# Kernel tuning notes

Measured on AMD Instinct MI355X. Metric: run time of the kernel, lower is better.

The kernel has to match this reference:

```python
import jax, jax.numpy as jnp
import numpy as np

EMBED = 2048
HEADS = 16
DFF = 4 * EMBED
EPS = 1e-5


def layernorm(x, g, b):
    mu = jnp.mean(x, axis=-1, keepdims=True)
    var = jnp.var(x, axis=-1, keepdims=True)
    return (x - mu) * jax.lax.rsqrt(var + EPS) * g + b


def setup_inputs() -> dict:
    key = jax.random.key(0)
    ks = jax.random.split(key, 16)
    s = 1.0 / np.sqrt(EMBED)
    sf = 1.0 / np.sqrt(DFF)
    return {
        "x": jax.random.normal(ks[0], (2, 2048, EMBED), jnp.float32),
        "Wq": jax.random.normal(ks[1], (EMBED, EMBED), jnp.float32) * s,
        "bq": jnp.zeros((EMBED,), jnp.float32),
        "Wk": jax.random.normal(ks[2], (EMBED, EMBED), jnp.float32) * s,
        "bk": jnp.zeros((EMBED,), jnp.float32),
        "Wv": jax.random.normal(ks[3], (EMBED, EMBED), jnp.float32) * s,
        "bv": jnp.zeros((EMBED,), jnp.float32),
        "Wo": jax.random.normal(ks[4], (EMBED, EMBED), jnp.float32) * s,
        "bo": jnp.zeros((EMBED,), jnp.float32),
        "g1": jnp.ones((EMBED,), jnp.float32),
        "b1": jnp.zeros((EMBED,), jnp.float32),
        "g2": jnp.ones((EMBED,), jnp.float32),
        "b2": jnp.zeros((EMBED,), jnp.float32),
        "W1": jax.random.normal(ks[5], (EMBED, DFF), jnp.float32) * s,
        "bf1": jnp.zeros((DFF,), jnp.float32),
        "W2": jax.random.normal(ks[6], (DFF, EMBED), jnp.float32) * sf,
        "bf2": jnp.zeros((EMBED,), jnp.float32),
    }


def reference(x, Wq, bq, Wk, bk, Wv, bv, Wo, bo, g1, b1, g2, b2, W1, bf1, W2, bf2):
    B, N, C = x.shape
    H = HEADS
    hd = C // H
    # QKV projections -> [B, H, N, hd]
    def split_heads(t):
        return t.reshape(B, N, H, hd).transpose(0, 2, 1, 3)
    q = split_heads(x @ Wq + bq)
    k = split_heads(x @ Wk + bk)
    v = split_heads(x @ Wv + bv)
    # scores [B, H, N, N]
    attn = jnp.einsum('bhqd,bhkd->bhqk', q, k) / np.sqrt(hd)
    attn = jax.nn.softmax(attn, axis=-1)
    out = jnp.einsum('bhqk,bhkd->bhqd', attn, v)
    out = out.transpose(0, 2, 1, 3).reshape(B, N, C)
    out = out @ Wo + bo
    h = layernorm(x + out, g1, b1)
    ff = jax.nn.gelu(h @ W1 + bf1, approximate=False) @ W2 + bf2
    return layernorm(h + ff, g2, b2)
```

## Files before the change

kernel.cpp:

```cpp
#include <hip/hip_runtime.h>
#include <math.h>

#define EMBED 2048
#define DFF   8192
#define TOK   4096
#define SEQ   2048
#define HEADS 16
#define HD    128
#define LDQ   6144

typedef __attribute__((ext_vector_type(8))) short short8;
typedef __attribute__((ext_vector_type(4))) float f32x4;

__device__ __forceinline__ unsigned short f2bf(float f) {
    unsigned int u = __float_as_uint(f);
    return (unsigned short)((u + 0x7FFFu + ((u >> 16) & 1u)) >> 16);
}
__device__ __forceinline__ float bf2f(unsigned short s) {
    return __uint_as_float(((unsigned int)s) << 16);
}
__device__ __forceinline__ float exp2_fast(float x) {
    return __builtin_amdgcn_exp2f(x);
}

__device__ __forceinline__ void async16(const void* g, void* l) {
    __builtin_amdgcn_global_load_lds((const __attribute__((address_space(1))) void*)g,
                                     (__attribute__((address_space(3))) void*)l, 16, 0, 0);
}

__device__ __forceinline__ float gelu_fast(float v) {
    const float y = 1.5957691216057308f * (v + 0.044715f * v * v * v);
    return v / (1.0f + __expf(-y));
}

template<int MODE>
__global__ __launch_bounds__(256, 2)
void gemm_bf16(const unsigned short* __restrict__ A, const unsigned short* __restrict__ B,
               const float* __restrict__ bias, const void* __restrict__ resid,
               unsigned short* __restrict__ C, int M, int N, int K, int lda)
{
    __shared__ __align__(16) float smemf[8448];
    unsigned short* As = (unsigned short*)smemf;
    unsigned short* Bs = As + 8192;
    float* Cs = smemf;

    const int t = threadIdx.x;
    const int w = t >> 6, l = t & 63;
    const int quad = l >> 4, m16 = l & 15;
    const long bm = (long)blockIdx.y * 128, bn = (long)blockIdx.x * 128;
    const int wr = (w >> 1)*64, wc = (w & 1)*64;

    f32x4 acc[4][4] = {};

    const int srow = w*16 + (l >> 2);
    const int sslot = l & 3;
    const unsigned short* Ag = A + (size_t)bm*lda;
    const unsigned short* Bg = B + (size_t)bn*K;

#pragma unroll
    for (int u = 0; u < 2; ++u) {
        const int row = u*64 + srow;
        const int c = sslot ^ ((row >> 1) & 3);
        async16(Ag + (size_t)row*lda + c*8, &As[u*2048 + w*512]);
        async16(Bg + (size_t)row*K   + c*8, &Bs[u*2048 + w*512]);
    }

    const int iters = K >> 5;
    for (int it = 0; it < iters; ++it) {
        __syncthreads();
        if (it + 1 < iters) {
            const int k0 = (it + 1) << 5;
            const int bo = ((it + 1) & 1) * 4096;
#pragma unroll
            for (int u = 0; u < 2; ++u) {
                const int row = u*64 + srow;
                const int c = sslot ^ ((row >> 1) & 3);
                async16(Ag + (size_t)row*lda + k0 + c*8, &As[bo + u*2048 + w*512]);
                async16(Bg + (size_t)row*K   + k0 + c*8, &Bs[bo + u*2048 + w*512]);
            }
        }
        const int co = (it & 1) * 4096;
        short8 af[4], bf[4];
#pragma unroll
        for (int s = 0; s < 4; ++s) {
            const int ra = wr + s*16 + m16;
            const int sla = quad ^ ((ra >> 1) & 3);
            af[s] = *(const short8*)&As[co + ra*32 + sla*8];
            const int rb = wc + s*16 + m16;
            const int slb = quad ^ ((rb >> 1) & 3);
            bf[s] = *(const short8*)&Bs[co + rb*32 + slb*8];
        }
#pragma unroll
        for (int ms = 0; ms < 4; ++ms)
#pragma unroll
            for (int ns = 0; ns < 4; ++ns)
                acc[ms][ns] = __builtin_amdgcn_mfma_f32_16x16x32_bf16(af[ms], bf[ns], acc[ms][ns], 0, 0, 0);
    }

    const int ecol = (t & 15) * 8;
    float bias8[8];
#pragma unroll
    for (int i = 0; i < 8; ++i) bias8[i] = bias[bn + ecol + i];

#pragma unroll
    for (int pass = 0; pass < 2; ++pass) {
        __syncthreads();
        if ((w >> 1) == pass) {
#pragma unroll
            for (int ms = 0; ms < 4; ++ms)
#pragma unroll
                for (int ns = 0; ns < 4; ++ns)
#pragma unroll
                    for (int r = 0; r < 4; ++r)
                        Cs[(ms*16 + quad*4 + r)*132 + wc + ns*16 + m16] = acc[ms][ns][r];
        }
        __syncthreads();
#pragma unroll
        for (int j = 0; j < 4; ++j) {
            const int row = j*16 + (t >> 4);
            float v[8];
            *(f32x4*)&v[0] = *(const f32x4*)&Cs[row*132 + ecol];
            *(f32x4*)&v[4] = *(const f32x4*)&Cs[row*132 + ecol + 4];
            const long gr = bm + pass*64 + row;
            const long go = gr*N + bn + ecol;
            float r8[8];
            if (MODE == 1) {
                *(f32x4*)&r8[0] = *(const f32x4*)((const float*)resid + go);
                *(f32x4*)&r8[4] = *(const f32x4*)((const float*)resid + go + 4);
            }
            short8 rb16;
            if (MODE == 3) rb16 = *(const short8*)((const unsigned short*)resid + go);
            short8 o;
#pragma unroll
            for (int i = 0; i < 8; ++i) {
                float y = v[i] + bias8[i];
                if (MODE == 1) y += r8[i];
                if (MODE == 3) y += bf2f((unsigned short)rb16[i]);
                if (MODE == 2) y = gelu_fast(y);
                o[i] = (short)f2bf(y);
            }
            *(short8*)&C[go] = o;
        }
    }
}

__global__ __launch_bounds__(256, 2)
void attn_flash(unsigned short* __restrict__ qkv)
{
    __shared__ unsigned short Ks2[2][64*128];
    __shared__ unsigned short Vt2[2][128*72];
    __shared__ unsigned short Ps[4*16*72];

    const int t = threadIdx.x;
    const int w = t >> 6, l = t & 63;
    const int quad = l >> 4, m16 = l & 15;

    const int dd = blockIdx.x;
    const int bh = (dd & 7)*4 + ((dd >> 3) >> 5);
    const int qt = (dd >> 3) & 31;
    const int b = bh >> 4, h = bh & 15;

    const long rowq = (long)b*SEQ + qt*64;
    const long rowb = (long)b*SEQ;
    const int qc = h*HD;
    const int kc = EMBED + h*HD;
    const int vc = 2*EMBED + h*HD;

    const int rbase = w*4 + (l >> 4);
    const int slot  = l & 15;
    const int vslot = t & 15;
    const int vrp   = t >> 4;

    unsigned short* Qs = Ks2[1];

    short8 va[2], vb[2];
#pragma unroll
    for (int u = 0; u < 2; ++u) {
        const int rp = u*16 + vrp;
        va[u] = *(const short8*)(qkv + (rowb + 2*rp    )*LDQ + vc + vslot*8);
        vb[u] = *(const short8*)(qkv + (rowb + 2*rp + 1)*LDQ + vc + vslot*8);
    }
#pragma unroll
    for (int u = 0; u < 4; ++u) {
        const int row = u*16 + rbase;
        const int c = slot ^ ((row >> 1) & 7);
        async16(qkv + (rowq + row)*LDQ + qc + c*8, Qs + u*2048 + w*512);
        async16(qkv + (rowb + row)*LDQ + kc + c*8, &Ks2[0][u*2048 + w*512]);
    }
#pragma unroll
    for (int u = 0; u < 2; ++u) {
        const int rp = u*16 + vrp;
#pragma unroll
        for (int i = 0; i < 8; ++i) {
            const int dv = vslot*8 + i;
            const int col = (2*rp) ^ (((dv >> 5) & 3) << 3);
            unsigned int pv = (unsigned int)(unsigned short)va[u][i] |
                              ((unsigned int)(unsigned short)vb[u][i] << 16);
            *(unsigned int*)&Vt2[0][dv*72 + col] = pv;
        }
    }
    __syncthreads();

    short8 af[4];
#pragma unroll
    for (int ks = 0; ks < 4; ++ks) {
        const int row = w*16 + m16;
        const int sl = (4*ks + quad) ^ ((row >> 1) & 7);
        af[ks] = *(const short8*)&Qs[row*128 + sl*8];
    }
    __syncthreads();

    f32x4 O[8] = {};
    float mrun[4] = {-1e30f,-1e30f,-1e30f,-1e30f};
    float lrun[4] = {0.f,0.f,0.f,0.f};
    unsigned short* Pw = Ps + w*16*72;
    const float SC = 0.08838834764831845f * 1.4426950408889634f;

    for (int kt = 0; kt < SEQ/64; ++kt) {
        const int cur = kt & 1;
        const bool pre = (kt + 1 < SEQ/64);
        const long rowkv = rowb + (long)(kt + 1)*64;

        if (pre) {
#pragma unroll
            for (int u = 0; u < 2; ++u) {
                const int rp = u*16 + vrp;
                va[u] = *(const short8*)(qkv + (rowkv + 2*rp    )*LDQ + vc + vslot*8);
                vb[u] = *(const short8*)(qkv + (rowkv + 2*rp + 1)*LDQ + vc + vslot*8);
            }
#pragma unroll
            for (int u = 0; u < 4; ++u) {
                const int row = u*16 + rbase;
                const int c = slot ^ ((row >> 1) & 7);
                async16(qkv + (rowkv + row)*LDQ + kc + c*8, &Ks2[cur^1][u*2048 + w*512]);
            }
        }

        f32x4 S[4];
#pragma unroll
        for (int ns = 0; ns < 4; ++ns) {
            f32x4 a = {0.f,0.f,0.f,0.f};
            const int row = ns*16 + m16;
            const int swr = (row >> 1) & 7;
#pragma unroll
            for (int ks = 0; ks < 4; ++ks) {
                const int sl = (4*ks + quad) ^ swr;
                const short8 bfr = *(const short8*)&Ks2[cur][row*128 + sl*8];
                a = __builtin_amdgcn_mfma_f32_16x16x32_bf16(af[ks], bfr, a, 0, 0, 0);
            }
#pragma unroll
            for (int r = 0; r < 4; ++r) a[r] *= SC;
            S[ns] = a;
        }

        float al[4], rs[4];
#pragma unroll
        for (int r = 0; r < 4; ++r) {
            float tm = fmaxf(fmaxf(S[0][r], S[1][r]), fmaxf(S[2][r], S[3][r]));
            tm = fmaxf(tm, __shfl_xor(tm, 1));
            tm = fmaxf(tm, __shfl_xor(tm, 2));
            tm = fmaxf(tm, __shfl_xor(tm, 4));
            tm = fmaxf(tm, __shfl_xor(tm, 8));
            const float mn = fmaxf(mrun[r], tm);
            al[r] = exp2_fast(mrun[r] - mn);
            mrun[r] = mn;
            rs[r] = 0.f;
        }
#pragma unroll
        for (int ns = 0; ns < 4; ++ns)
#pragma unroll
            for (int r = 0; r < 4; ++r) {
                const float p = exp2_fast(S[ns][r] - mrun[r]);
                rs[r] += p;
                Pw[(quad*4 + r)*72 + ns*16 + m16] = f2bf(p);
            }
#pragma unroll
        for (int r = 0; r < 4; ++r) {
            rs[r] += __shfl_xor(rs[r], 1);
            rs[r] += __shfl_xor(rs[r], 2);
            rs[r] += __shfl_xor(rs[r], 4);
            rs[r] += __shfl_xor(rs[r], 8);
            lrun[r] = lrun[r]*al[r] + rs[r];
        }
        if (__any((al[0] != 1.f) | (al[1] != 1.f) | (al[2] != 1.f) | (al[3] != 1.f))) {
#pragma unroll
            for (int i = 0; i < 8; ++i)
#pragma unroll
                for (int r = 0; r < 4; ++r) O[i][r] *= al[r];
        }

        if (pre) {
#pragma unroll
            for (int u = 0; u < 2; ++u) {
                const int rp = u*16 + vrp;
#pragma unroll
                for (int i = 0; i < 8; ++i) {
                    const int dv = vslot*8 + i;
                    const int col = (2*rp) ^ (((dv >> 5) & 3) << 3);
                    unsigned int pv = (unsigned int)(unsigned short)va[u][i] |
                                      ((unsigned int)(unsigned short)vb[u][i] << 16);
                    *(unsigned int*)&Vt2[cur^1][dv*72 + col] = pv;
                }
            }
        }

#pragma unroll
        for (int ks2 = 0; ks2 < 2; ++ks2) {
            const short8 ap = *(const short8*)&Pw[m16*72 + ks2*32 + quad*8];
#pragma unroll
            for (int ds = 0; ds < 8; ++ds) {
                const int dv = ds*16 + m16;
                const int jcol = (ks2*32 + quad*8) ^ (((dv >> 5) & 3) << 3);
                const short8 bv = *(const short8*)&Vt2[cur][dv*72 + jcol];
                O[ds] = __builtin_amdgcn_mfma_f32_16x16x32_bf16(ap, bv, O[ds], 0, 0, 0);
            }
        }

        __syncthreads();
    }

    float inv[4];
#pragma unroll
    for (int r = 0; r < 4; ++r) inv[r] = 1.0f / lrun[r];
#pragma unroll
    for (int ds = 0; ds < 8; ++ds)
#pragma unroll
        for (int r = 0; r < 4; ++r) {
            const long row = rowq + w*16 + quad*4 + r;
            qkv[row*LDQ + qc + ds*16 + m16] = f2bf(O[ds][r] * inv[r]);
        }
}

template<int OUTF32>
__global__ __launch_bounds__(256)
void ln_bf16(const unsigned short* __restrict__ X, const float* __restrict__ g,
             const float* __restrict__ be, void* __restrict__ Y)
{
    __shared__ float r1[256], r2[256];
    const int t = threadIdx.x;
    const long row = blockIdx.x;
    const unsigned short* x = X + row*EMBED;
    float v[8];
    const short8 xv = *(const short8*)(x + t*8);
    float s = 0.f, s2 = 0.f;
#pragma unroll
    for (int i = 0; i < 8; ++i) {
        v[i] = bf2f((unsigned short)xv[i]);
        s += v[i]; s2 += v[i]*v[i];
    }
    r1[t] = s; r2[t] = s2;
    __syncthreads();
    for (int k = 128; k > 0; k >>= 1) {
        if (t < k) { r1[t] += r1[t+k]; r2[t] += r2[t+k]; }
        __syncthreads();
    }
    const float mu = r1[0] * (1.0f/EMBED);
    const float var = r2[0] * (1.0f/EMBED) - mu*mu;
    const float rstd = rsqrtf(var + 1e-5f);
    if (OUTF32) {
        float* y = (float*)Y + row*EMBED + t*8;
#pragma unroll
        for (int i = 0; i < 8; ++i) y[i] = (v[i]-mu)*rstd*g[t*8+i] + be[t*8+i];
    } else {
        unsigned short* y = (unsigned short*)Y + row*EMBED;
        short8 o;
#pragma unroll
        for (int i = 0; i < 8; ++i) o[i] = (short)f2bf((v[i]-mu)*rstd*g[t*8+i] + be[t*8+i]);
        *(short8*)(y + t*8) = o;
    }
}

__global__ __launch_bounds__(256)
void cvt_transpose(const float* __restrict__ W, unsigned short* __restrict__ Wt, int K, int N)
{
    __shared__ unsigned short T[32][33];
    const int t = threadIdx.x;
    const long n0 = (long)blockIdx.x*32, k0 = (long)blockIdx.y*32;
    {
        const int r = t >> 3, c = (t & 7)*4;
        const float4 vv = *(const float4*)&W[(k0 + r)*N + n0 + c];
        T[r][c+0] = f2bf(vv.x); T[r][c+1] = f2bf(vv.y);
        T[r][c+2] = f2bf(vv.z); T[r][c+3] = f2bf(vv.w);
    }
    __syncthreads();
    const int rn = t >> 3, kk = (t & 7)*4;
    unsigned int p0 = (unsigned int)T[kk+0][rn] | ((unsigned int)T[kk+1][rn] << 16);
    unsigned int p1 = (unsigned int)T[kk+2][rn] | ((unsigned int)T[kk+3][rn] << 16);
    unsigned int* dst = (unsigned int*)&Wt[(n0 + rn)*K + k0 + kk];
    dst[0] = p0; dst[1] = p1;
}

__global__ __launch_bounds__(256)
void cvt_f32_bf16(const float* __restrict__ X, unsigned short* __restrict__ Y, long n)
{
    const long i = ((long)blockIdx.x*256 + threadIdx.x)*8;
    if (i >= n) return;
    const float4 a = *(const float4*)&X[i];
    const float4 b = *(const float4*)&X[i+4];
    short8 o;
    o[0]=(short)f2bf(a.x); o[1]=(short)f2bf(a.y); o[2]=(short)f2bf(a.z); o[3]=(short)f2bf(a.w);
    o[4]=(short)f2bf(b.x); o[5]=(short)f2bf(b.y); o[6]=(short)f2bf(b.z); o[7]=(short)f2bf(b.w);
    *(short8*)&Y[i] = o;
}

__global__ __launch_bounds__(256)
void concat_bias(const float* __restrict__ bq, const float* __restrict__ bk,
                 const float* __restrict__ bv, float* __restrict__ out)
{
    const int i = blockIdx.x*256 + threadIdx.x;
    if (i < 2048) out[i] = bq[i];
    else if (i < 4096) out[i] = bk[i-2048];
    else if (i < 6144) out[i] = bv[i-4096];
}

extern "C" void kernel_launch(void* const* d_in, const int* in_sizes, int n_in,
                              void* d_out, int out_size, void* d_ws, size_t ws_size,
                              hipStream_t stream)
{
    const float* x   = (const float*)d_in[0];
    const float* Wq  = (const float*)d_in[1];
    const float* bq  = (const float*)d_in[2];
    const float* Wk  = (const float*)d_in[3];
    const float* bk  = (const float*)d_in[4];
    const float* Wv  = (const float*)d_in[5];
    const float* bv  = (const float*)d_in[6];
    const float* Wo  = (const float*)d_in[7];
    const float* bo  = (const float*)d_in[8];
    const float* g1  = (const float*)d_in[9];
    const float* b1  = (const float*)d_in[10];
    const float* g2v = (const float*)d_in[11];
    const float* b2v = (const float*)d_in[12];
    const float* W1  = (const float*)d_in[13];
    const float* bf1 = (const float*)d_in[14];
    const float* W2  = (const float*)d_in[15];
    const float* bf2 = (const float*)d_in[16];
    float* out = (float*)d_out;

    char* ws = (char*)d_ws;
    unsigned short* Wqkvt = (unsigned short*)(ws + 0);
    unsigned short* Wot   = (unsigned short*)(ws + 25165824);
    unsigned short* W1t   = (unsigned short*)(ws + 33554432);
    unsigned short* W2t   = (unsigned short*)(ws + 67108864);
    float*          bqkv  = (float*)         (ws + 100663296);
    char* arenaA = ws + 100687872;
    unsigned short* xb   = (unsigned short*)(arenaA);
    unsigned short* qkv  = (unsigned short*)(arenaA + 16777216);
    unsigned short* res1 = (unsigned short*)(arenaA);
    unsigned short* ff   = (unsigned short*)(arenaA);
    unsigned short* hb   = (unsigned short*)(ws + 167796736);
    unsigned short* res2 = (unsigned short*)(ws + 0);

    const dim3 blk(256);

    cvt_transpose<<<dim3(64,64),  blk, 0, stream>>>(Wq, Wqkvt,             2048, 2048);
    cvt_transpose<<<dim3(64,64),  blk, 0, stream>>>(Wk, Wqkvt + 2048*2048, 2048, 2048);
    cvt_transpose<<<dim3(64,64),  blk, 0, stream>>>(Wv, Wqkvt + 2*2048*2048, 2048, 2048);
    cvt_transpose<<<dim3(64,64),  blk, 0, stream>>>(Wo, Wot, 2048, 2048);
    cvt_transpose<<<dim3(256,64), blk, 0, stream>>>(W1, W1t, 2048, 8192);
    cvt_transpose<<<dim3(64,256), blk, 0, stream>>>(W2, W2t, 8192, 2048);
    concat_bias<<<dim3(24), blk, 0, stream>>>(bq, bk, bv, bqkv);
    cvt_f32_bf16<<<dim3(4096), blk, 0, stream>>>(x, xb, (long)TOK*EMBED);

    gemm_bf16<0><<<dim3(48,32), blk, 0, stream>>>(xb, Wqkvt, bqkv, nullptr, qkv, TOK, 6144, 2048, 2048);
    attn_flash<<<dim3(1024), blk, 0, stream>>>(qkv);
    gemm_bf16<1><<<dim3(16,32), blk, 0, stream>>>(qkv, Wot, bo, x, res1, TOK, 2048, 2048, 6144);
    ln_bf16<0><<<dim3(4096), blk, 0, stream>>>(res1, g1, b1, hb);
    gemm_bf16<2><<<dim3(64,32), blk, 0, stream>>>(hb, W1t, bf1, nullptr, ff, TOK, 8192, 2048, 2048);
    gemm_bf16<3><<<dim3(16,32), blk, 0, stream>>>(ff, W2t, bf2, hb, res2, TOK, 2048, 8192, 8192);
    ln_bf16<1><<<dim3(4096), blk, 0, stream>>>(res2, g2v, b2v, out);
}
```

Baseline: 956.0 us.

## Process 128 query rows per attention block to reuse K/V tiles

Each attention block now handles 128 query rows instead of 64, with each wave computing two 16-row query slices against the same K and V tiles, which halves the grid to 512 blocks. Q is staged through the Vt2 buffer at startup. The aim is to halve global K/V loads and V transposes per query and amortize LDS reads of K/V across two MFMA chains. The cost is more accumulator registers (two O sets), which may lower occupancy, and fewer blocks, which may underfill the 256 CUs.

```diff
diff --git a/kernel.cpp b/kernel.cpp
--- a/kernel.cpp
+++ b/kernel.cpp
@@ -156,11 +156,11 @@
     const int quad = l >> 4, m16 = l & 15;
 
     const int dd = blockIdx.x;
-    const int bh = (dd & 7)*4 + ((dd >> 3) >> 5);
-    const int qt = (dd >> 3) & 31;
+    const int bh = (dd & 7)*4 + ((dd >> 3) >> 4);
+    const int qt = (dd >> 3) & 15;
     const int b = bh >> 4, h = bh & 15;
 
-    const long rowq = (long)b*SEQ + qt*64;
+    const long rowq = (long)b*SEQ + qt*128;
     const long rowb = (long)b*SEQ;
     const int qc = h*HD;
     const int kc = EMBED + h*HD;
@@ -171,7 +171,7 @@
     const int vslot = t & 15;
     const int vrp   = t >> 4;
 
-    unsigned short* Qs = Ks2[1];
+    unsigned short* QsOv = (unsigned short*)Vt2;
 
     short8 va[2], vb[2];
 #pragma unroll
@@ -181,12 +181,30 @@
         vb[u] = *(const short8*)(qkv + (rowb + 2*rp + 1)*LDQ + vc + vslot*8);
     }
 #pragma unroll
+    for (int u = 0; u < 8; ++u) {
+        const int row = u*16 + rbase;
+        const int c = slot ^ ((row >> 1) & 7);
+        async16(qkv + (rowq + row)*LDQ + qc + c*8, QsOv + u*2048 + w*512);
+    }
+#pragma unroll
     for (int u = 0; u < 4; ++u) {
         const int row = u*16 + rbase;
         const int c = slot ^ ((row >> 1) & 7);
-        async16(qkv + (rowq + row)*LDQ + qc + c*8, Qs + u*2048 + w*512);
         async16(qkv + (rowb + row)*LDQ + kc + c*8, &Ks2[0][u*2048 + w*512]);
     }
+    __syncthreads();
+
+    short8 af[2][4];
+#pragma unroll
+    for (int qh = 0; qh < 2; ++qh)
+#pragma unroll
+        for (int ks = 0; ks < 4; ++ks) {
+            const int row = w*32 + qh*16 + m16;
+            const int sl = (4*ks + quad) ^ ((row >> 1) & 7);
+            af[qh][ks] = *(const short8*)&QsOv[row*128 + sl*8];
+        }
+    __syncthreads();
+
 #pragma unroll
     for (int u = 0; u < 2; ++u) {
         const int rp = u*16 + vrp;
@@ -201,18 +219,12 @@
     }
     __syncthreads();
 
-    short8 af[4];
-#pragma unroll
-    for (int ks = 0; ks < 4; ++ks) {
-        const int row = w*16 + m16;
-        const int sl = (4*ks + quad) ^ ((row >> 1) & 7);
-        af[ks] = *(const short8*)&Qs[row*128 + sl*8];
-    }
-    __syncthreads();
-
-    f32x4 O[8] = {};
-    float mrun[4] = {-1e30f,-1e30f,-1e30f,-1e30f};
-    float lrun[4] = {0.f,0.f,0.f,0.f};
+    f32x4 O[2][8] = {};
+    float mrun[2][4], lrun[2][4];
+#pragma unroll
+    for (int qh = 0; qh < 2; ++qh)
+#pragma unroll
+        for (int r = 0; r < 4; ++r) { mrun[qh][r] = -1e30f; lrun[qh][r] = 0.f; }
     unsigned short* Pw = Ps + w*16*72;
     const float SC = 0.08838834764831845f * 1.4426950408889634f;
 
@@ -236,99 +248,107 @@
             }
         }
 
-        f32x4 S[4];
+        f32x4 S[2][4];
 #pragma unroll
         for (int ns = 0; ns < 4; ++ns) {
-            f32x4 a = {0.f,0.f,0.f,0.f};
+            f32x4 a0 = {0.f,0.f,0.f,0.f}, a1 = {0.f,0.f,0.f,0.f};
             const int row = ns*16 + m16;
             const int swr = (row >> 1) & 7;
 #pragma unroll
             for (int ks = 0; ks < 4; ++ks) {
                 const int sl = (4*ks + quad) ^ swr;
                 const short8 bfr = *(const short8*)&Ks2[cur][row*128 + sl*8];
-                a = __builtin_amdgcn_mfma_f32_16x16x32_bf16(af[ks], bfr, a, 0, 0, 0);
-            }
-#pragma unroll
-            for (int r = 0; r < 4; ++r) a[r] *= SC;
-            S[ns] = a;
-        }
-
-        float al[4], rs[4];
-#pragma unroll
-        for (int r = 0; r < 4; ++r) {
-            float tm = fmaxf(fmaxf(S[0][r], S[1][r]), fmaxf(S[2][r], S[3][r]));
-            tm = fmaxf(tm, __shfl_xor(tm, 1));
-            tm = fmaxf(tm, __shfl_xor(tm, 2));
-            tm = fmaxf(tm, __shfl_xor(tm, 4));
-            tm = fmaxf(tm, __shfl_xor(tm, 8));
-            const float mn = fmaxf(mrun[r], tm);
-            al[r] = exp2_fast(mrun[r] - mn);
-            mrun[r] = mn;
-            rs[r] = 0.f;
-        }
-#pragma unroll
-        for (int ns = 0; ns < 4; ++ns)
+                a0 = __builtin_amdgcn_mfma_f32_16x16x32_bf16(af[0][ks], bfr, a0, 0, 0, 0);
+                a1 = __builtin_amdgcn_mfma_f32_16x16x32_bf16(af[1][ks], bfr, a1, 0, 0, 0);
+            }
+#pragma unroll
+            for (int r = 0; r < 4; ++r) { a0[r] *= SC; a1[r] *= SC; }
+            S[0][ns] = a0; S[1][ns] = a1;
+        }
+
+#pragma unroll
+        for (int qh = 0; qh < 2; ++qh) {
+            float al[4], rs4[4];
 #pragma unroll
             for (int r = 0; r < 4; ++r) {
-                const float p = exp2_fast(S[ns][r] - mrun[r]);
-                rs[r] += p;
-                Pw[(quad*4 + r)*72 + ns*16 + m16] = f2bf(p);
-            }
-#pragma unroll
-        for (int r = 0; r < 4; ++r) {
-            rs[r] += __shfl_xor(rs[r], 1);
-            rs[r] += __shfl_xor(rs[r], 2);
-            rs[r] += __shfl_xor(rs[r], 4);
-            rs[r] += __shfl_xor(rs[r], 8);
-            lrun[r] = lrun[r]*al[r] + rs[r];
-        }
-        if (__any((al[0] != 1.f) | (al[1] != 1.f) | (al[2] != 1.f) | (al[3] != 1.f))) {
-#pragma unroll
-            for (int i = 0; i < 8; ++i)
-#pragma unroll
-                for (int r = 0; r < 4; ++r) O[i][r] *= al[r];
-        }
-
-        if (pre) {
-#pragma unroll
-            for (int u = 0; u < 2; ++u) {
-                const int rp = u*16 + vrp;
-#pragma unroll
-                for (int i = 0; i < 8; ++i) {
-                    const int dv = vslot*8 + i;
-                    const int col = (2*rp) ^ (((dv >> 5) & 3) << 3);
-                    unsigned int pv = (unsigned int)(unsigned short)va[u][i] |
-                                      ((unsigned int)(unsigned short)vb[u][i] << 16);
-                    *(unsigned int*)&Vt2[cur^1][dv*72 + col] = pv;
+                float tm = fmaxf(fmaxf(S[qh][0][r], S[qh][1][r]), fmaxf(S[qh][2][r], S[qh][3][r]));
+                tm = fmaxf(tm, __shfl_xor(tm, 1));
+                tm = fmaxf(tm, __shfl_xor(tm, 2));
+                tm = fmaxf(tm, __shfl_xor(tm, 4));
+                tm = fmaxf(tm, __shfl_xor(tm, 8));
+                const float mn = fmaxf(mrun[qh][r], tm);
+                al[r] = exp2_fast(mrun[qh][r] - mn);
+                mrun[qh][r] = mn;
+                rs4[r] = 0.f;
+            }
+#pragma unroll
+            for (int ns = 0; ns < 4; ++ns)
+#pragma unroll
+                for (int r = 0; r < 4; ++r) {
+                    const float p = exp2_fast(S[qh][ns][r] - mrun[qh][r]);
+                    rs4[r] += p;
+                    Pw[(quad*4 + r)*72 + ns*16 + m16] = f2bf(p);
                 }
-            }
-        }
-
-#pragma unroll
-        for (int ks2 = 0; ks2 < 2; ++ks2) {
-            const short8 ap = *(const short8*)&Pw[m16*72 + ks2*32 + quad*8];
-#pragma unroll
-            for (int ds = 0; ds < 8; ++ds) {
-                const int dv = ds*16 + m16;
-                const int jcol = (ks2*32 + quad*8) ^ (((dv >> 5) & 3) << 3);
-                const short8 bv = *(const short8*)&Vt2[cur][dv*72 + jcol];
-                O[ds] = __builtin_amdgcn_mfma_f32_16x16x32_bf16(ap, bv, O[ds], 0, 0, 0);
+#pragma unroll
+            for (int r = 0; r < 4; ++r) {
+                rs4[r] += __shfl_xor(rs4[r], 1);
+                rs4[r] += __shfl_xor(rs4[r], 2);
+                rs4[r] += __shfl_xor(rs4[r], 4);
+                rs4[r] += __shfl_xor(rs4[r], 8);
+                lrun[qh][r] = lrun[qh][r]*al[r] + rs4[r];
+            }
+            if (__any((al[0] != 1.f) | (al[1] != 1.f) | (al[2] != 1.f) | (al[3] != 1.f))) {
+#pragma unroll
+                for (int i = 0; i < 8; ++i)
+#pragma unroll
+                    for (int r = 0; r < 4; ++r) O[qh][i][r] *= al[r];
+            }
+
+            if (qh == 1 && pre) {
+#pragma unroll
+                for (int u = 0; u < 2; ++u) {
+                    const int rp = u*16 + vrp;
+#pragma unroll
+                    for (int i = 0; i < 8; ++i) {
+                        const int dv = vslot*8 + i;
+                        const int col = (2*rp) ^ (((dv >> 5) & 3) << 3);
+                        unsigned int pv = (unsigned int)(unsigned short)va[u][i] |
+                                          ((unsigned int)(unsigned short)vb[u][i] << 16);
+                        *(unsigned int*)&Vt2[cur^1][dv*72 + col] = pv;
+                    }
+                }
+            }
+
+#pragma unroll
+            for (int ks2 = 0; ks2 < 2; ++ks2) {
+                const short8 ap = *(const short8*)&Pw[m16*72 + ks2*32 + quad*8];
+#pragma unroll
+                for (int ds = 0; ds < 8; ++ds) {
+                    const int dv = ds*16 + m16;
+                    const int jcol = (ks2*32 + quad*8) ^ (((dv >> 5) & 3) << 3);
+                    const short8 bv = *(const short8*)&Vt2[cur][dv*72 + jcol];
+                    O[qh][ds] = __builtin_amdgcn_mfma_f32_16x16x32_bf16(ap, bv, O[qh][ds], 0, 0, 0);
+                }
             }
         }
 
         __syncthreads();
     }
 
-    float inv[4];
-#pragma unroll
-    for (int r = 0; r < 4; ++r) inv[r] = 1.0f / lrun[r];
-#pragma unroll
-    for (int ds = 0; ds < 8; ++ds)
-#pragma unroll
-        for (int r = 0; r < 4; ++r) {
-            const long row = rowq + w*16 + quad*4 + r;
-            qkv[row*LDQ + qc + ds*16 + m16] = f2bf(O[ds][r] * inv[r]);
-        }
+    float inv[2][4];
+#pragma unroll
+    for (int qh = 0; qh < 2; ++qh)
+#pragma unroll
+        for (int r = 0; r < 4; ++r) inv[qh][r] = 1.0f / lrun[qh][r];
+#pragma unroll
+    for (int qh = 0; qh < 2; ++qh)
+#pragma unroll
+        for (int ds = 0; ds < 8; ++ds)
+#pragma unroll
+            for (int r = 0; r < 4; ++r) {
+                const long row = rowq + w*32 + qh*16 + quad*4 + r;
+                qkv[row*LDQ + qc + ds*16 + m16] = f2bf(O[qh][ds][r] * inv[qh][r]);
+            }
 }
 
 template<int OUTF32>
@@ -462,7 +482,7 @@
     cvt_f32_bf16<<<dim3(4096), blk, 0, stream>>>(x, xb, (long)TOK*EMBED);
 
     gemm_bf16<0><<<dim3(48,32), blk, 0, stream>>>(xb, Wqkvt, bqkv, nullptr, qkv, TOK, 6144, 2048, 2048);
-    attn_flash<<<dim3(1024), blk, 0, stream>>>(qkv);
+    attn_flash<<<dim3(512), blk, 0, stream>>>(qkv);
     gemm_bf16<1><<<dim3(16,32), blk, 0, stream>>>(qkv, Wot, bo, x, res1, TOK, 2048, 2048, 6144);
     ln_bf16<0><<<dim3(4096), blk, 0, stream>>>(res1, g1, b1, hb);
     gemm_bf16<2><<<dim3(64,32), blk, 0, stream>>>(hb, W1t, bf1, nullptr, ff, TOK, 8192, 2048, 2048);
```

After: 929.8 us. 2.7% less time.
